# Kernel optimization log

Measured on AMD Instinct MI355X. Metric: run time of the kernel, lower is better.

Reference implementation:

```python
import jax, jax.numpy as jnp
import numpy as np

GS = 256      # grid/node count
PARAM = 128   # feature width
KC = 32       # keepconst (constant features)
I1, I2 = 64, 32
PK = PARAM - KC
K_DIV = 16.0  # neighbor-count normalizer
EPS = 1e-3    # Keras BatchNorm default epsilon
B = 4


def _bn(x, g, b, m, v):
    # inference-mode batch norm over last axis
    return (x - m) * jax.lax.rsqrt(v + EPS) * g + b


def setup_inputs() -> dict:
    key = jax.random.key(0)
    ks = jax.random.split(key, 24)
    mat = (jax.random.uniform(ks[0], (B, GS, GS)) < (K_DIV / GS)).astype(jnp.float32)
    val = jax.random.normal(ks[1], (B, GS, PARAM), dtype=jnp.float32)
    def w(k, shape):
        fan = shape[0] if len(shape) > 1 else shape[0]
        return jax.random.normal(k, shape, dtype=jnp.float32) * (1.0 / np.sqrt(fan))
    inp = {
        'mat': mat, 'val': val,
        'M1': w(ks[2], (2 * PARAM, I1)), 'B1': 0.05 * jax.random.normal(ks[3], (I1,)),
        'M2': w(ks[4], (I1, I2)),        'B2': 0.05 * jax.random.normal(ks[5], (I2,)),
        'M3': w(ks[6], (I2, PK)),        'B3': 0.05 * jax.random.normal(ks[7], (PK,)),
    }
    for idx, d in zip((1, 2, 3), (I1, I2, PK)):
        kk = jax.random.split(ks[7 + idx], 4)
        inp[f'g{idx}'] = 1.0 + 0.1 * jax.random.normal(kk[0], (d,), dtype=jnp.float32)
        inp[f'b{idx}'] = 0.1 * jax.random.normal(kk[1], (d,), dtype=jnp.float32)
        inp[f'm{idx}'] = 0.1 * jax.random.normal(kk[2], (d,), dtype=jnp.float32)
        inp[f'v{idx}'] = jax.random.uniform(kk[3], (d,), dtype=jnp.float32, minval=0.5, maxval=1.5)
    return inp


def reference(mat, val, M1, B1, M2, B2, M3, B3,
              g1, b1, m1, v1, g2, b2, m2, v2, g3, b3, m3, v3):
    con = val[:, :, :KC]
    # selector matmuls == gather: pair i -> (a=i//GS, b=i%GS)
    feat = jnp.repeat(val, GS, axis=1)          # (B, GS*GS, PARAM) = val_a
    vb = jnp.tile(val, (1, GS, 1))              # (B, GS*GS, PARAM) = val_b
    premlp = jnp.concatenate([feat, vb - feat], axis=-1)  # (B, GS*GS, 2*PARAM)
    s = jax.nn.relu(_bn(premlp @ M1 + B1, g1, b1, m1, v1))
    s = jax.nn.relu(_bn(s @ M2 + B2, g2, b2, m2, v2))
    s = jax.nn.relu(_bn(s @ M3 + B3, g3, b3, m3, v3))      # (B, GS*GS, PK)
    res = s.reshape(val.shape[0], GS, GS, PK)               # (B, a, b, PK)
    # masked scatter-sum over neighbor axis b
    summ = jnp.einsum('babk,bab->bak'.replace('a', 'x').replace('b', 'y', 1), res, mat) if False else \
        jnp.einsum('bxyk,bxy->bxk', res, mat)               # (B, GS, PK)
    var = jnp.clip(summ / K_DIV, -1.0, 1.0)                 # advrelu([-1,1]) == clip
    return jnp.concatenate([con, var], axis=-1)             # (B, GS, PARAM)
```

## Files before the change

kernel.cpp:

```cpp
#include <hip/hip_runtime.h>

#define GS    256
#define PARAM 128
#define KC    32
#define I1    64
#define I2    32
#define PK    96
#define B_    4
#define NROWS (B_ * GS)
#define EPS   1e-3f
#define KDIV_INV (1.0f / 16.0f)

constexpr int U_OFF   = 0;
constexpr int W_OFF   = NROWS * I1;
constexpr int M2F_OFF = 2 * NROWS * I1;
constexpr int C2_OFF  = M2F_OFF + I1 * I2;
constexpr int M3F_OFF = C2_OFF + I2;
constexpr int C3_OFF  = M3F_OFF + I2 * PK;
constexpr int C1_OFF  = C3_OFF + PK;

__global__ __launch_bounds__(256) void glmlp_precompute(
    const float* __restrict__ val, const float* __restrict__ M1,
    const float* __restrict__ B1,
    const float* __restrict__ M2, const float* __restrict__ B2,
    const float* __restrict__ M3, const float* __restrict__ B3,
    const float* __restrict__ g1, const float* __restrict__ b1,
    const float* __restrict__ m1, const float* __restrict__ v1,
    const float* __restrict__ g2, const float* __restrict__ b2,
    const float* __restrict__ m2, const float* __restrict__ v2,
    const float* __restrict__ g3, const float* __restrict__ b3,
    const float* __restrict__ m3, const float* __restrict__ v3,
    float* __restrict__ ws, float* __restrict__ out)
{
    const int blk = blockIdx.x;
    const int t = threadIdx.x;

    if (blk < NROWS) {
        __shared__ float vrow[PARAM];
        __shared__ float red[4][I1];
        const int r = blk;
        if (t < PARAM) vrow[t] = val[r * PARAM + t];
        if (t < KC) out[r * PARAM + t] = val[r * PARAM + t];
        __syncthreads();

        const int i = t & (I1 - 1);
        const int q = t >> 6;
        const float* __restrict__ Mb = M1 + ((q >> 1) ? (PARAM * I1) : 0);
        const int p0 = (q & 1) * 64;
        float aa = 0.f, bb = 0.f;
        #pragma unroll 8
        for (int p = 0; p < 64; p += 2) {
            aa = fmaf(vrow[p0 + p],     Mb[(p0 + p) * I1 + i],     aa);
            bb = fmaf(vrow[p0 + p + 1], Mb[(p0 + p + 1) * I1 + i], bb);
        }
        red[q][i] = aa + bb;
        __syncthreads();

        if (q == 0) {
            const float T  = red[0][i] + red[1][i];
            const float Wv = red[2][i] + red[3][i];
            const float s1 = g1[i] * rsqrtf(v1[i] + EPS);
            ws[U_OFF + r * I1 + i] = (T - Wv) * s1;
            ws[W_OFF + r * I1 + i] = Wv * s1;
        }
    } else {
        if (t < I1) {
            const float s1 = g1[t] * rsqrtf(v1[t] + EPS);
            ws[C1_OFF + t] = B1[t] * s1 + b1[t] - m1[t] * s1;
        }
        if (t < I2) {
            const float s2 = g2[t] * rsqrtf(v2[t] + EPS);
            ws[C2_OFF + t] = B2[t] * s2 + b2[t] - m2[t] * s2;
        }
        if (t < PK) {
            const float s3 = g3[t] * rsqrtf(v3[t] + EPS);
            ws[C3_OFF + t] = B3[t] * s3 + b3[t] - m3[t] * s3;
        }
        for (int idx = t; idx < I1 * I2; idx += 256) {
            const int j = idx & (I2 - 1);
            const float s2 = g2[j] * rsqrtf(v2[j] + EPS);
            ws[M2F_OFF + idx] = M2[idx] * s2;
        }
        for (int idx = t; idx < I2 * PK; idx += 256) {
            const int k = idx % PK;
            const float s3 = g3[k] * rsqrtf(v3[k] + EPS);
            ws[M3F_OFF + idx] = M3[idx] * s3;
        }
    }
}

__global__ __launch_bounds__(256) void glmlp_pairs(
    const float* __restrict__ mat, const float* __restrict__ ws,
    float* __restrict__ out)
{
    __shared__ float m2s[I1 * I2];
    __shared__ float m3s[I2 * PK];
    __shared__ float uxs[I1];
    __shared__ float c2s[I2];
    __shared__ float c3s[PK];
    __shared__ float partial[4][PK];
    __shared__ int   acty[GS];
    __shared__ int   cnt;

    const int r = blockIdx.x;
    const int t = threadIdx.x;
    const int lane = t & 63;
    const int w = t >> 6;
    const int jj = lane & 31;
    const int p0 = (lane >> 5) * 32;
    const int wbase = r & ~(GS - 1);
    const float* __restrict__ W = ws + W_OFF;

    if (t == 0) cnt = 0;
    const float mv = mat[r * GS + t];
    for (int idx = t; idx < I1 * I2; idx += 256) m2s[idx] = ws[M2F_OFF + idx];
    for (int idx = t; idx < I2 * PK; idx += 256) m3s[idx] = ws[M3F_OFF + idx];
    if (t < I2) c2s[t] = ws[C2_OFF + t];
    if (t < PK) c3s[t] = ws[C3_OFF + t];
    if (t < I1) uxs[t] = ws[U_OFF + r * I1 + t] + ws[C1_OFF + t];
    __syncthreads();

    if (mv != 0.0f) acty[atomicAdd(&cnt, 1)] = t;
    __syncthreads();
    const int n = cnt;

    const float ux   = uxs[lane];
    const float c2j  = c2s[jj];
    const float c3_0 = c3s[lane];
    const float c3_1 = c3s[64 + jj];

    float acc0 = 0.f, acc1 = 0.f;

    int p = w;
    float wv = (p < n) ? W[(wbase + acty[p]) * I1 + lane] : 0.f;
    while (p < n) {
        const int pn = p + 4;
        const float wvn = (pn < n) ? W[(wbase + acty[pn]) * I1 + lane] : 0.f;

        const float h1 = fmaxf(ux + wv, 0.f);

        float a = 0.f, b = 0.f;
        #pragma unroll
        for (int s = 0; s < 32; s += 2) {
            a = fmaf(__shfl(h1, p0 + s),     m2s[(p0 + s) * I2 + jj],     a);
            b = fmaf(__shfl(h1, p0 + s + 1), m2s[(p0 + s + 1) * I2 + jj], b);
        }
        const float ab = a + b;
        const float h2 = fmaxf(__shfl(ab, jj) + __shfl(ab, 32 + jj) + c2j, 0.f);

        float d0a = c3_0, d0b = 0.f, d1a = c3_1, d1b = 0.f;
        #pragma unroll
        for (int i = 0; i < I2; i += 2) {
            const float he = __shfl(h2, i);
            const float ho = __shfl(h2, i + 1);
            d0a = fmaf(he, m3s[i * PK + lane], d0a);
            d0b = fmaf(ho, m3s[(i + 1) * PK + lane], d0b);
            d1a = fmaf(he, m3s[i * PK + 64 + jj], d1a);
            d1b = fmaf(ho, m3s[(i + 1) * PK + 64 + jj], d1b);
        }
        acc0 += fmaxf(d0a + d0b, 0.f);
        acc1 += fmaxf(d1a + d1b, 0.f);

        wv = wvn;
        p = pn;
    }

    partial[w][lane] = acc0;
    if (lane < 32) partial[w][64 + lane] = acc1;
    __syncthreads();

    if (t < PK) {
        float v = (partial[0][t] + partial[1][t] + partial[2][t] + partial[3][t])
                  * KDIV_INV;
        v = fminf(fmaxf(v, -1.0f), 1.0f);
        out[r * PARAM + KC + t] = v;
    }
}

extern "C" void kernel_launch(void* const* d_in, const int* in_sizes, int n_in,
                              void* d_out, int out_size, void* d_ws, size_t ws_size,
                              hipStream_t stream) {
    const float* mat = (const float*)d_in[0];
    const float* val = (const float*)d_in[1];
    const float* M1  = (const float*)d_in[2];
    const float* B1  = (const float*)d_in[3];
    const float* M2  = (const float*)d_in[4];
    const float* B2  = (const float*)d_in[5];
    const float* M3  = (const float*)d_in[6];
    const float* B3  = (const float*)d_in[7];
    const float* g1  = (const float*)d_in[8];
    const float* b1  = (const float*)d_in[9];
    const float* m1  = (const float*)d_in[10];
    const float* v1  = (const float*)d_in[11];
    const float* g2  = (const float*)d_in[12];
    const float* b2  = (const float*)d_in[13];
    const float* m2  = (const float*)d_in[14];
    const float* v2  = (const float*)d_in[15];
    const float* g3  = (const float*)d_in[16];
    const float* b3  = (const float*)d_in[17];
    const float* m3  = (const float*)d_in[18];
    const float* v3  = (const float*)d_in[19];

    float* ws  = (float*)d_ws;
    float* out = (float*)d_out;

    hipLaunchKernelGGL(glmlp_precompute, dim3(NROWS + 1), dim3(256), 0, stream,
                       val, M1, B1, M2, B2, M3, B3,
                       g1, b1, m1, v1, g2, b2, m2, v2, g3, b3, m3, v3,
                       ws, out);

    hipLaunchKernelGGL(glmlp_pairs, dim3(NROWS), dim3(256), 0, stream,
                       mat, ws, out);
}
```

Before: 122.7 us.

## Keep MLP weights in registers and broadcast activations with readlane

Weights for layers two and three are now loaded into per-thread registers straight from the workspace instead of being staged in shared memory. The shuffle-based broadcasts are replaced with v_readlane scalar broadcasts. The layer-2 reduction is restructured so each lane computes a full 64-term dot product, which removes the split-half combine shuffles. This removes LDS traffic and cross-lane permute latency from the inner pair loop, at the cost of about 130 extra VGPRs per thread, which may reduce occupancy, and redundant global loads of the weights in every block.

New measurement: 109.8 us. 1.12x faster.

```diff
diff --git a/kernel.cpp b/kernel.cpp
--- a/kernel.cpp
+++ b/kernel.cpp
@@ -18,6 +18,10 @@
 constexpr int M3F_OFF = C2_OFF + I2;
 constexpr int C3_OFF  = M3F_OFF + I2 * PK;
 constexpr int C1_OFF  = C3_OFF + PK;
+
+__device__ __forceinline__ float rdlane(float v, int l) {
+    return __uint_as_float(__builtin_amdgcn_readlane(__float_as_uint(v), l));
+}
 
 __global__ __launch_bounds__(256) void glmlp_precompute(
     const float* __restrict__ val, const float* __restrict__ M1,
@@ -93,13 +97,8 @@
     const float* __restrict__ mat, const float* __restrict__ ws,
     float* __restrict__ out)
 {
-    __shared__ float m2s[I1 * I2];
-    __shared__ float m3s[I2 * PK];
-    __shared__ float uxs[I1];
-    __shared__ float c2s[I2];
-    __shared__ float c3s[PK];
+    __shared__ int   acty[GS];
     __shared__ float partial[4][PK];
-    __shared__ int   acty[GS];
     __shared__ int   cnt;
 
     const int r = blockIdx.x;
@@ -107,27 +106,31 @@
     const int lane = t & 63;
     const int w = t >> 6;
     const int jj = lane & 31;
-    const int p0 = (lane >> 5) * 32;
     const int wbase = r & ~(GS - 1);
     const float* __restrict__ W = ws + W_OFF;
 
     if (t == 0) cnt = 0;
     const float mv = mat[r * GS + t];
-    for (int idx = t; idx < I1 * I2; idx += 256) m2s[idx] = ws[M2F_OFF + idx];
-    for (int idx = t; idx < I2 * PK; idx += 256) m3s[idx] = ws[M3F_OFF + idx];
-    if (t < I2) c2s[t] = ws[C2_OFF + t];
-    if (t < PK) c3s[t] = ws[C3_OFF + t];
-    if (t < I1) uxs[t] = ws[U_OFF + r * I1 + t] + ws[C1_OFF + t];
+
+    float m2col[I1];
+    #pragma unroll
+    for (int s = 0; s < I1; ++s)
+        m2col[s] = ws[M2F_OFF + s * I2 + jj];
+    float m3a[I2], m3b[I2];
+    #pragma unroll
+    for (int i = 0; i < I2; ++i) {
+        m3a[i] = ws[M3F_OFF + i * PK + lane];
+        m3b[i] = ws[M3F_OFF + i * PK + 64 + jj];
+    }
+    const float ux  = ws[U_OFF + r * I1 + lane] + ws[C1_OFF + lane];
+    const float c2j = ws[C2_OFF + jj];
+    const float c30 = ws[C3_OFF + lane];
+    const float c31 = ws[C3_OFF + 64 + jj];
+
     __syncthreads();
-
     if (mv != 0.0f) acty[atomicAdd(&cnt, 1)] = t;
     __syncthreads();
     const int n = cnt;
-
-    const float ux   = uxs[lane];
-    const float c2j  = c2s[jj];
-    const float c3_0 = c3s[lane];
-    const float c3_1 = c3s[64 + jj];
 
     float acc0 = 0.f, acc1 = 0.f;
 
@@ -139,24 +142,25 @@
 
         const float h1 = fmaxf(ux + wv, 0.f);
 
-        float a = 0.f, b = 0.f;
+        float a0 = 0.f, a1 = 0.f, a2 = 0.f, a3 = 0.f;
         #pragma unroll
-        for (int s = 0; s < 32; s += 2) {
-            a = fmaf(__shfl(h1, p0 + s),     m2s[(p0 + s) * I2 + jj],     a);
-            b = fmaf(__shfl(h1, p0 + s + 1), m2s[(p0 + s + 1) * I2 + jj], b);
-        }
-        const float ab = a + b;
-        const float h2 = fmaxf(__shfl(ab, jj) + __shfl(ab, 32 + jj) + c2j, 0.f);
-
-        float d0a = c3_0, d0b = 0.f, d1a = c3_1, d1b = 0.f;
+        for (int s = 0; s < I1; s += 4) {
+            a0 = fmaf(rdlane(h1, s + 0), m2col[s + 0], a0);
+            a1 = fmaf(rdlane(h1, s + 1), m2col[s + 1], a1);
+            a2 = fmaf(rdlane(h1, s + 2), m2col[s + 2], a2);
+            a3 = fmaf(rdlane(h1, s + 3), m2col[s + 3], a3);
+        }
+        const float h2 = fmaxf((a0 + a1) + (a2 + a3) + c2j, 0.f);
+
+        float d0a = c30, d0b = 0.f, d1a = c31, d1b = 0.f;
         #pragma unroll
         for (int i = 0; i < I2; i += 2) {
-            const float he = __shfl(h2, i);
-            const float ho = __shfl(h2, i + 1);
-            d0a = fmaf(he, m3s[i * PK + lane], d0a);
-            d0b = fmaf(ho, m3s[(i + 1) * PK + lane], d0b);
-            d1a = fmaf(he, m3s[i * PK + 64 + jj], d1a);
-            d1b = fmaf(ho, m3s[(i + 1) * PK + 64 + jj], d1b);
+            const float he = rdlane(h2, i);
+            const float ho = rdlane(h2, i + 1);
+            d0a = fmaf(he, m3a[i],     d0a);
+            d0b = fmaf(ho, m3a[i + 1], d0b);
+            d1a = fmaf(he, m3b[i],     d1a);
+            d1b = fmaf(ho, m3b[i + 1], d1b);
         }
         acc0 += fmaxf(d0a + d0b, 0.f);
         acc1 += fmaxf(d1a + d1b, 0.f);
```
